# Kernel tuning notes

Hardware: AMD Instinct MI355X
Metric: run time of the kernel (lower is better)

Reference implementation:

```python
import jax, jax.numpy as jnp
import numpy as np

HEADS, DQK, DV = 4, 128, 128
HH, WW = 32, 32
SCALE = DQK ** -0.5
EPS = 1e-5


def bn(x, g, b, m, v):
    # eval-mode BatchNorm2d over channel dim of NCHW
    inv = g * jax.lax.rsqrt(v + EPS)
    return x * inv[:, None, None] + (b - m * inv)[:, None, None]


def rel_to_abs(x):
    # x: (B, Nh, L, 2L-1) -> (B, Nh, L, L)
    B, Nh, L, _ = x.shape
    x = jnp.pad(x, ((0, 0), (0, 0), (0, 0), (0, 1)))
    fx = x.reshape(B, Nh, L * 2 * L)
    fx = jnp.pad(fx, ((0, 0), (0, 0), (0, L - 1)))
    fx = fx.reshape(B, Nh, L + 1, 2 * L - 1)
    return fx[:, :, :L, L - 1:]


def rel_logits_1d(q, rel_k):
    # q: (B, Nh, H, W, D); rel_k: (2W-1, D)
    B, Nh, H, W, D = q.shape
    r = jnp.einsum('bnhwd,rd->bnhwr', q, rel_k)
    r = rel_to_abs(r.reshape(B, Nh * H, W, 2 * W - 1))
    r = r.reshape(B, Nh, H, W, W)
    return jnp.broadcast_to(r[:, :, :, None], (B, Nh, H, H, W, W))


def pos_bias(q, rel_h, rel_w):
    # q: (B, Nh, H*W, D), already scaled
    B, Nh, L, D = q.shape
    q5 = q.reshape(B, Nh, HH, WW, D)
    rw = rel_logits_1d(q5, rel_w)                     # (B,N,H,Hx,W,W)
    rw = rw.transpose(0, 1, 2, 4, 3, 5).reshape(B, Nh, HH * WW, HH * WW)
    rh = rel_logits_1d(q5.transpose(0, 1, 3, 2, 4), rel_h)  # (B,N,W,Wx,H,H)
    rh = rh.transpose(0, 1, 4, 2, 5, 3).reshape(B, Nh, HH * WW, HH * WW)
    return rw + rh


def to_heads(x):
    # (B, Nh*d, H, W) -> (B, Nh, H*W, d)
    B, C, H, W = x.shape
    x = x.reshape(B, HEADS, C // HEADS, H, W)
    return x.transpose(0, 1, 3, 4, 2).reshape(B, HEADS, H * W, C // HEADS)


def mhsa(x, w_qk, w_v, rel_h, rel_w):
    B, C, H, W = x.shape
    qk = jnp.einsum('bchw,oc->bohw', x, w_qk)
    q, k = jnp.split(qk, 2, axis=1)
    v = jnp.einsum('bchw,oc->bohw', x, w_v)
    q, k, v = to_heads(q), to_heads(k), to_heads(v)
    q = q * SCALE
    logits = jnp.einsum('bnid,bnjd->bnij', q, k) + pos_bias(q, rel_h, rel_w)
    weights = jax.nn.softmax(logits, axis=-1)
    out = jnp.einsum('bnij,bnjd->bnid', weights, v)   # (B,Nh,HW,dv)
    out = out.reshape(B, HEADS, H, W, DV).transpose(0, 1, 4, 2, 3)
    return out.reshape(B, HEADS * DV, H, W)


def setup_inputs() -> dict:
    key = jax.random.key(0)
    ks = jax.random.split(key, 12)
    d = {
        'x': jax.random.normal(ks[0], (8, 512, HH, WW), jnp.float32),
        'w_qk': jax.random.normal(ks[1], (2 * HEADS * DQK, 512), jnp.float32) * 0.02,
        'w_v': jax.random.normal(ks[2], (HEADS * DV, 512), jnp.float32) * 0.02,
        'rel_h': jax.random.normal(ks[3], (2 * HH - 1, DQK), jnp.float32) * SCALE,
        'rel_w': jax.random.normal(ks[4], (2 * WW - 1, DQK), jnp.float32) * SCALE,
        'g1': jnp.ones((512,), jnp.float32),
        'b1': jnp.zeros((512,), jnp.float32),
        'm1': jax.random.normal(ks[5], (512,), jnp.float32) * 0.1,
        'v1': jax.random.uniform(ks[6], (512,), jnp.float32) + 0.5,
        'g2': jnp.ones((512,), jnp.float32),
        'b2': jnp.zeros((512,), jnp.float32),
        'm2': jax.random.normal(ks[7], (512,), jnp.float32) * 0.1,
        'v2': jax.random.uniform(ks[8], (512,), jnp.float32) + 0.5,
        'w_fc': jax.random.normal(ks[9], (512, 512, 3, 3), jnp.float32) * 0.02,
        'bias_fc': jnp.zeros((512,), jnp.float32),
    }
    return d


def reference(x, w_qk, w_v, rel_h, rel_w, g1, b1, m1, v1, g2, b2, m2, v2, w_fc, bias_fc):
    out = jax.nn.relu(bn(x, g1, b1, m1, v1))
    out = mhsa(out, w_qk, w_v, rel_h, rel_w)
    x = out + x
    out = jax.nn.relu(bn(x, g2, b2, m2, v2))
    out = jax.lax.conv_general_dilated(
        out, w_fc, window_strides=(1, 1), padding='SAME',
        dimension_numbers=('NCHW', 'OIHW', 'NCHW')) + bias_fc[:, None, None]
    return out + x
```

## Files before the change

### kernel.cpp

```cpp
#include <hip/hip_runtime.h>

typedef __bf16 v8bf __attribute__((ext_vector_type(8)));
typedef float f32x4 __attribute__((ext_vector_type(4)));

#define DEVI static __device__ __forceinline__

DEVI v8bf load8(const __bf16* p) { return *reinterpret_cast<const v8bf*>(p); }

DEVI f32x4 mfma16(v8bf a, v8bf b, f32x4 c) {
  return __builtin_amdgcn_mfma_f32_16x16x32_bf16(a, b, c, 0, 0, 0);
}

DEVI void gld16(const __bf16* g, __bf16* l) {
  __builtin_amdgcn_global_load_lds(
      (const __attribute__((address_space(1))) unsigned int*)(const void*)g,
      (__attribute__((address_space(3))) unsigned int*)(void*)l, 16, 0, 0);
}

#define SCALE_Q 0.08838834764831845f

__global__ void k_prep(const float* __restrict__ wqk, const float* __restrict__ wv,
                       const float* __restrict__ relh, const float* __restrict__ relw,
                       const float* __restrict__ wfc, __bf16* __restrict__ wqkb,
                       __bf16* __restrict__ wvb, __bf16* __restrict__ rhb,
                       __bf16* __restrict__ rwb, __bf16* __restrict__ Wt,
                       float* __restrict__ zpad4) {
  const int bid = blockIdx.x, tid = threadIdx.x;
  if (bid < 2048) {
    int i = bid * 256 + tid;
    wqkb[i] = (__bf16)wqk[i];
  } else if (bid < 3072) {
    int i = (bid - 2048) * 256 + tid;
    wvb[i] = (__bf16)wv[i];
  } else if (bid < 3104) {
    int i = (bid - 3072) * 256 + tid;
    if (i < 8064) rhb[i] = (__bf16)relh[i];
  } else if (bid < 3136) {
    int i = (bid - 3104) * 256 + tid;
    if (i < 8064) rwb[i] = (__bf16)relw[i];
  } else if (bid < 4160) {
    int i = (bid - 3136) * 256 + tid;
    const float* src = wfc + (size_t)i * 9;
#pragma unroll
    for (int tap = 0; tap < 9; ++tap)
      Wt[(size_t)tap * 262144 + i] = (__bf16)src[tap];
  } else {
    int i = (bid - 4160) * 256 + tid;
    f32x4 z = {0.f, 0.f, 0.f, 0.f};
    reinterpret_cast<f32x4*>(zpad4)[i] = z;
  }
}

__global__ void k_bn1(const float* __restrict__ x, const float* __restrict__ g,
                      const float* __restrict__ bb, const float* __restrict__ m,
                      const float* __restrict__ v, __bf16* __restrict__ y) {
  __shared__ float tile[32][33];
  const int b = blockIdx.z, c0 = blockIdx.y * 32, s0 = blockIdx.x * 32;
  const int tx = threadIdx.x, ty = threadIdx.y;
#pragma unroll
  for (int r = 0; r < 4; ++r) {
    int c = c0 + ty + r * 8;
    float inv = g[c] * rsqrtf(v[c] + 1e-5f);
    float beta = bb[c] - m[c] * inv;
    float val = x[((size_t)b * 512 + c) * 1024 + s0 + tx] * inv + beta;
    tile[ty + r * 8][tx] = fmaxf(val, 0.0f);
  }
  __syncthreads();
#pragma unroll
  for (int r = 0; r < 4; ++r) {
    int s = s0 + ty + r * 8;
    y[((size_t)b * 1024 + s) * 512 + c0 + tx] = (__bf16)tile[tx][ty + r * 8];
  }
}

__global__ void k_bn2c(float* o0x2, const float* __restrict__ o1,
                       const float* __restrict__ lp, const float* __restrict__ xin,
                       const float* __restrict__ g, const float* __restrict__ bb,
                       const float* __restrict__ m, const float* __restrict__ v,
                       __bf16* __restrict__ zp) {
  __shared__ float tile[32][33];
  const int b = blockIdx.z, c0 = blockIdx.y * 32, s0 = blockIdx.x * 32;
  const int tx = threadIdx.x, ty = threadIdx.y;
  const int bnrow = b * 4 + (c0 >> 7);
  const int scol = s0 + tx;
  const float linv =
      1.0f / (lp[bnrow * 1024 + scol] + lp[32768 + bnrow * 1024 + scol]);
#pragma unroll
  for (int r = 0; r < 4; ++r) {
    int c = c0 + ty + r * 8;
    float inv = g[c] * rsqrtf(v[c] + 1e-5f);
    float beta = bb[c] - m[c] * inv;
    size_t idx = ((size_t)b * 512 + c) * 1024 + scol;
    float t = (o0x2[idx] + o1[idx]) * linv + xin[idx];
    o0x2[idx] = t;
    tile[ty + r * 8][tx] = fmaxf(t * inv + beta, 0.0f);
  }
  __syncthreads();
#pragma unroll
  for (int r = 0; r < 4; ++r) {
    int s = s0 + ty + r * 8;
    int hh = s >> 5, ww = s & 31;
    zp[(((size_t)b * 34 + hh + 1) * 34 + ww + 1) * 512 + c0 + tx] =
        (__bf16)tile[tx][ty + r * 8];
  }
}

__global__ __launch_bounds__(256) void k_proj(
    const __bf16* __restrict__ wall, const __bf16* __restrict__ y,
    __bf16* __restrict__ qout, __bf16* __restrict__ kout,
    __bf16* __restrict__ vout) {
  __shared__ __bf16 As[2][128 * 32];
  __shared__ __bf16 Bs[2][128 * 32];
  const int t = threadIdx.x;
  const int wave = t >> 6, lane = t & 63;
  const int l15 = lane & 15, quad = lane >> 4;
  const int mbase = blockIdx.x * 128;
  const int nbase = blockIdx.y * 128;
  const int mh = (wave >> 1) * 64, nh = (wave & 1) * 64;
  const bool isv = mbase >= 1024;

  const int row0 = t >> 2, part8 = (t & 3) * 8;
  const __bf16* gA0 = wall + (size_t)(mbase + row0) * 512 + part8;
  const __bf16* gA1 = gA0 + (size_t)64 * 512;
  const __bf16* gB0 = y + (size_t)(nbase + row0) * 512 + part8;
  const __bf16* gB1 = gB0 + (size_t)64 * 512;
  const int wofs = wave * 512;

  const f32x4 fz = {0.f, 0.f, 0.f, 0.f};
  f32x4 acc[4][4];
#pragma unroll
  for (int i = 0; i < 4; ++i)
#pragma unroll
    for (int j = 0; j < 4; ++j) acc[i][j] = fz;

  gld16(gA0, &As[0][wofs]);
  gld16(gA1, &As[0][2048 + wofs]);
  gld16(gB0, &Bs[0][wofs]);
  gld16(gB1, &Bs[0][2048 + wofs]);
  __syncthreads();

#pragma unroll 1
  for (int r = 0; r < 16; ++r) {
    const int cur = r & 1;
    if (r < 15) {
      const int kn = (r + 1) * 32;
      gld16(gA0 + kn, &As[cur ^ 1][wofs]);
      gld16(gA1 + kn, &As[cur ^ 1][2048 + wofs]);
      gld16(gB0 + kn, &Bs[cur ^ 1][wofs]);
      gld16(gB1 + kn, &Bs[cur ^ 1][2048 + wofs]);
    }
    v8bf a[4], bfr[4];
#pragma unroll
    for (int i = 0; i < 4; ++i)
      a[i] = load8(&As[cur][(mh + i * 16 + l15) * 32 + quad * 8]);
#pragma unroll
    for (int j = 0; j < 4; ++j)
      bfr[j] = load8(&Bs[cur][(nh + j * 16 + l15) * 32 + quad * 8]);
    if (isv) {
#pragma unroll
      for (int i = 0; i < 4; ++i)
#pragma unroll
        for (int j = 0; j < 4; ++j) acc[i][j] = mfma16(a[i], bfr[j], acc[i][j]);
    } else {
#pragma unroll
      for (int i = 0; i < 4; ++i)
#pragma unroll
        for (int j = 0; j < 4; ++j) acc[i][j] = mfma16(bfr[j], a[i], acc[i][j]);
    }
    __syncthreads();
  }

  if (isv) {
#pragma unroll
    for (int i = 0; i < 4; ++i)
#pragma unroll
      for (int j = 0; j < 4; ++j)
#pragma unroll
        for (int r = 0; r < 4; ++r) {
          int o = mbase + mh + i * 16 + quad * 4 + r;
          int nflat = nbase + nh + j * 16 + l15;
          int b = nflat >> 10, s = nflat & 1023;
          int oe = o - 1024; int n = oe >> 7, d = oe & 127;
          vout[(((size_t)b * 4 + n) * 128 + d) * 1024 + s] = (__bf16)acc[i][j][r];
        }
  } else {
    const bool isq = mbase < 512;
#pragma unroll
    for (int i = 0; i < 4; ++i)
#pragma unroll
      for (int j = 0; j < 4; ++j)
#pragma unroll
        for (int r = 0; r < 4; ++r) {
          int o = mbase + mh + i * 16 + l15;
          int nflat = nbase + nh + j * 16 + quad * 4 + r;
          int b = nflat >> 10, s = nflat & 1023;
          float val = acc[i][j][r];
          if (isq) {
            int n = o >> 7, d = o & 127;
            qout[(((size_t)b * 4 + n) * 1024 + s) * 128 + d] = (__bf16)(val * SCALE_Q);
          } else {
            int oe = o - 512; int n = oe >> 7, d = oe & 127;
            kout[(((size_t)b * 4 + n) * 1024 + s) * 128 + d] = (__bf16)val;
          }
        }
  }
}

__global__ __launch_bounds__(256, 2) void k_attn(
    const __bf16* __restrict__ q, const __bf16* __restrict__ kmat,
    const __bf16* __restrict__ vt, const __bf16* __restrict__ relh,
    const __bf16* __restrict__ relw, float* __restrict__ o0,
    float* __restrict__ o1, float* __restrict__ lpart) {
  __shared__ __bf16 Ks[32 * 128];
  __shared__ __bf16 Vs[128 * 32];
  __shared__ __bf16 P[4 * 32 * 36];
  __shared__ __bf16 RWs[128][33];
  __shared__ __bf16 RHs[128][33];

  const int Lb = blockIdx.x;
  const int xcd = Lb & 7, local = Lb >> 3;
  const int bn = xcd * 4 + (local & 3);
  const int qblk = (local >> 2) & 7;
  const int half = local >> 5;
  const int s0 = qblk * 128;

  const int t = threadIdx.x;
  const int wave = t >> 6, lane = t & 63;
  const int l15 = lane & 15, quad = lane >> 4;
  const size_t hoff = ((size_t)bn) << 17;
  const int s0w = s0 + wave * 32;
  const int h0w = s0w >> 5;
  const int j00 = half * 512;

  const __bf16* kgA =
      kmat + hoff + (size_t)((t >> 2) & 31) * 128 + (t >> 7) * 32 + (t & 3) * 8;
  const __bf16* vgA = vt + hoff + (size_t)(t >> 2) * 1024 + (t & 3) * 8;
  __bf16* kswA = Ks + wave * 512;
  __bf16* vswA = Vs + wave * 512;

#pragma unroll
  for (int c = 0; c < 2; ++c)
    gld16(kgA + (size_t)j00 * 128 + c * 64, kswA + c * 2048);
#pragma unroll
  for (int dh = 0; dh < 2; ++dh)
    gld16(vgA + (size_t)dh * 64 * 1024 + j00, vswA + dh * 2048);

  v8bf aq[2][4];
#pragma unroll
  for (int h = 0; h < 2; ++h) {
    const __bf16* qp = q + hoff + (size_t)(s0w + h * 16 + l15) * 128;
#pragma unroll
    for (int kk = 0; kk < 4; ++kk) aq[h][kk] = load8(qp + kk * 32 + quad * 8);
  }

#pragma unroll
  for (int h = 0; h < 2; ++h) {
#pragma unroll
    for (int nt = 0; nt < 4; ++nt) {
      int rr = nt * 16 + l15;
      const __bf16* bp = relw + (size_t)rr * 128;
      f32x4 acc = {0.f, 0.f, 0.f, 0.f};
#pragma unroll
      for (int kk = 0; kk < 4; ++kk)
        acc = mfma16(aq[h][kk], load8(bp + kk * 32 + quad * 8), acc);
#pragma unroll
      for (int r = 0; r < 4; ++r) {
        int row15 = quad * 4 + r;
        int wj = rr + h * 16 + row15 - 31;
        if (wj >= 0 && wj < 32)
          RWs[wave * 32 + h * 16 + row15][wj] = (__bf16)acc[r];
      }
    }
#pragma unroll
    for (int nt = 0; nt < 2; ++nt) {
      int hj = nt * 16 + l15;
      const __bf16* bp = relh + (size_t)(hj - h0w + 31) * 128;
      f32x4 acc = {0.f, 0.f, 0.f, 0.f};
#pragma unroll
      for (int kk = 0; kk < 4; ++kk)
        acc = mfma16(aq[h][kk], load8(bp + kk * 32 + quad * 8), acc);
#pragma unroll
      for (int r = 0; r < 4; ++r)
        RHs[wave * 32 + h * 16 + quad * 4 + r][hj] = (__bf16)acc[r];
    }
  }

  float rwreg[2][4][2];
#pragma unroll
  for (int h = 0; h < 2; ++h)
#pragma unroll
    for (int r = 0; r < 4; ++r) {
      const int gi = wave * 32 + h * 16 + quad * 4 + r;
      rwreg[h][r][0] = (float)RWs[gi][l15];
      rwreg[h][r][1] = (float)RWs[gi][l15 + 16];
    }

  __syncthreads();

  const f32x4 fz = {0.f, 0.f, 0.f, 0.f};
  float lsum[2][4];
#pragma unroll
  for (int h = 0; h < 2; ++h)
#pragma unroll
    for (int r = 0; r < 4; ++r) lsum[h][r] = 0.f;
  f32x4 oacc[2][8];
#pragma unroll
  for (int h = 0; h < 2; ++h)
#pragma unroll
    for (int dt = 0; dt < 8; ++dt) oacc[h][dt] = fz;
  __bf16* Pw = P + wave * 32 * 36;

#pragma unroll 1
  for (int iter = 0; iter < 16; ++iter) {
    asm volatile("s_waitcnt vmcnt(2)" ::: "memory");
    __builtin_amdgcn_s_barrier();
    __builtin_amdgcn_sched_barrier(0);

    v8bf kf[8];
#pragma unroll
    for (int nj = 0; nj < 2; ++nj)
#pragma unroll
      for (int kk = 0; kk < 4; ++kk)
        kf[nj * 4 + kk] =
            load8(&Ks[kk * 1024 + (nj * 16 + l15) * 32 + quad * 8]);

    f32x4 sacc[2][2];
    __builtin_amdgcn_s_setprio(1);
#pragma unroll
    for (int h = 0; h < 2; ++h)
#pragma unroll
      for (int nj = 0; nj < 2; ++nj) {
        f32x4 a = fz;
#pragma unroll
        for (int kk = 0; kk < 4; ++kk)
          a = mfma16(aq[h][kk], kf[nj * 4 + kk], a);
        sacc[h][nj] = a;
      }
    __builtin_amdgcn_s_setprio(0);

    const int hjb = half * 16 + iter;
#pragma unroll
    for (int h = 0; h < 2; ++h)
#pragma unroll
      for (int r = 0; r < 4; ++r) {
        const int row = h * 16 + quad * 4 + r;
        const float rh0 = (float)RHs[wave * 32 + row][hjb];
#pragma unroll
        for (int nj = 0; nj < 2; ++nj) {
          float val = sacc[h][nj][r] + rwreg[h][r][nj] + rh0;
          float p = __expf(fminf(val, 60.0f));
          lsum[h][r] += p;
          Pw[row * 36 + nj * 16 + l15] = (__bf16)p;
        }
      }
    v8bf pf[2];
#pragma unroll
    for (int h = 0; h < 2; ++h)
      pf[h] = *reinterpret_cast<const v8bf*>(&Pw[(h * 16 + l15) * 36 + quad * 8]);

    asm volatile("s_waitcnt vmcnt(0)" ::: "memory");
    __builtin_amdgcn_s_barrier();
    __builtin_amdgcn_sched_barrier(0);

    if (iter < 15) {
      const int jn = j00 + (iter + 1) * 32;
#pragma unroll
      for (int c = 0; c < 2; ++c)
        gld16(kgA + (size_t)jn * 128 + c * 64, kswA + c * 2048);
    }

    __builtin_amdgcn_s_setprio(1);
#pragma unroll
    for (int dt = 0; dt < 8; ++dt) {
      v8bf vf = load8(&Vs[(dt * 16 + l15) * 32 + quad * 8]);
#pragma unroll
      for (int h = 0; h < 2; ++h)
        oacc[h][dt] = mfma16(vf, pf[h], oacc[h][dt]);
    }
    __builtin_amdgcn_s_setprio(0);

    if (iter < 15) {
      asm volatile("s_waitcnt lgkmcnt(0)" ::: "memory");
      __builtin_amdgcn_s_barrier();
      __builtin_amdgcn_sched_barrier(0);
      const int jn = j00 + (iter + 1) * 32;
#pragma unroll
      for (int dh = 0; dh < 2; ++dh)
        gld16(vgA + (size_t)dh * 64 * 1024 + jn, vswA + dh * 2048);
    }
  }

#pragma unroll
  for (int h = 0; h < 2; ++h)
#pragma unroll
    for (int r = 0; r < 4; ++r) {
#pragma unroll
      for (int msk = 8; msk >= 1; msk >>= 1)
        lsum[h][r] += __shfl_xor(lsum[h][r], msk);
    }
  if (l15 == 0) {
#pragma unroll
    for (int h = 0; h < 2; ++h)
#pragma unroll
      for (int r = 0; r < 4; ++r)
        lpart[half * 32768 + bn * 1024 + s0w + h * 16 + quad * 4 + r] =
            lsum[h][r];
  }

  {
    float* op = half ? o1 : o0;
#pragma unroll
    for (int h = 0; h < 2; ++h) {
      const int s = s0w + h * 16 + l15;
#pragma unroll
      for (int dt = 0; dt < 8; ++dt)
#pragma unroll
        for (int r = 0; r < 4; ++r) {
          int d = dt * 16 + quad * 4 + r;
          op[((size_t)bn * 128 + d) * 1024 + s] = oacc[h][dt][r];
        }
    }
  }
}

__global__ __launch_bounds__(256, 2) void k_conv(
    const __bf16* __restrict__ Wt, const __bf16* __restrict__ zp,
    float* __restrict__ part) {
  __shared__ __bf16 As[4 * 128 * 32];
  __shared__ __bf16 Bs[4 * 128 * 32];
  const int t = threadIdx.x;
  const int wave = t >> 6, lane = t & 63;
  const int l15 = lane & 15, quad = lane >> 4;

  const int Lb = blockIdx.x;
  const int logical = (Lb & 7) * 64 + (Lb >> 3);
  const int combo = logical & 7;
  const int ot = combo >> 1, sp = combo & 1;
  const int nt = logical >> 3;
  const int mbase = ot * 128;
  const int nbase = nt * 128;
  const int cs = sp * 256;
  const int mh = (wave >> 1) * 64, nh = (wave & 1) * 64;

  const int row0 = t >> 2;
  const int part8 = (t & 3) * 8;
  const __bf16* gA0 = Wt + (size_t)(mbase + row0) * 512 + cs + part8;
  const __bf16* gA1 = gA0 + (size_t)64 * 512;
  const int n0 = nbase + row0;
  const int b0 = n0 >> 10, spn = n0 & 1023;
  const __bf16* gB0 =
      zp + ((size_t)(b0 * 34 + (spn >> 5) + 1) * 34 + (spn & 31) + 1) * 512 + cs + part8;
  const __bf16* gB1 = gB0 + (size_t)2 * 34 * 512;
  const int wofs = wave * 512;

  const f32x4 fz = {0.f, 0.f, 0.f, 0.f};
  f32x4 acc[4][4];
#pragma unroll
  for (int i = 0; i < 4; ++i)
#pragma unroll
    for (int j = 0; j < 4; ++j) acc[i][j] = fz;

#pragma unroll 1
  for (int tap = 0; tap < 9; ++tap) {
    const int dh = tap / 3 - 1, dw = tap % 3 - 1;
    const size_t aoff = (size_t)tap * 512 * 512;
    const int boff = (dh * 34 + dw) * 512;
#pragma unroll 1
    for (int k0 = 0; k0 < 256; k0 += 128) {
      __syncthreads();
#pragma unroll
      for (int c = 0; c < 4; ++c) {
        const int kq = k0 + c * 32;
        gld16(gA0 + aoff + kq, As + c * 4096 + wofs);
        gld16(gA1 + aoff + kq, As + c * 4096 + 2048 + wofs);
        gld16(gB0 + boff + kq, Bs + c * 4096 + wofs);
        gld16(gB1 + boff + kq, Bs + c * 4096 + 2048 + wofs);
      }
      __syncthreads();
#pragma unroll
      for (int c = 0; c < 4; ++c) {
        v8bf a[4], bfr[4];
#pragma unroll
        for (int i = 0; i < 4; ++i)
          a[i] = load8(&As[c * 4096 + (mh + i * 16 + l15) * 32 + quad * 8]);
#pragma unroll
        for (int j = 0; j < 4; ++j)
          bfr[j] = load8(&Bs[c * 4096 + (nh + j * 16 + l15) * 32 + quad * 8]);
#pragma unroll
        for (int i = 0; i < 4; ++i)
#pragma unroll
          for (int j = 0; j < 4; ++j) acc[i][j] = mfma16(a[i], bfr[j], acc[i][j]);
      }
    }
  }

  float* pout = part + (size_t)sp * 8 * 512 * 1024;
#pragma unroll
  for (int i = 0; i < 4; ++i)
#pragma unroll
    for (int j = 0; j < 4; ++j)
#pragma unroll
      for (int r = 0; r < 4; ++r) {
        int o = mbase + mh + i * 16 + quad * 4 + r;
        int nn = nbase + nh + j * 16 + l15;
        int bb2 = nn >> 10, s = nn & 1023;
        pout[((size_t)bb2 * 512 + o) * 1024 + s] = acc[i][j][r];
      }
}

__global__ void k_sum(const float* __restrict__ part, const float* __restrict__ bias,
                      const float* __restrict__ x2, float* __restrict__ out) {
  int i = blockIdx.x * 256 + threadIdx.x;
  int o = (i >> 8) & 511;
  f32x4 p0 = reinterpret_cast<const f32x4*>(part)[i];
  f32x4 p1 = reinterpret_cast<const f32x4*>(part + (size_t)8 * 512 * 1024)[i];
  f32x4 xr = reinterpret_cast<const f32x4*>(x2)[i];
  float bo = bias[o];
  f32x4 r;
#pragma unroll
  for (int c = 0; c < 4; ++c) r[c] = p0[c] + p1[c] + bo + xr[c];
  reinterpret_cast<f32x4*>(out)[i] = r;
}

extern "C" void kernel_launch(void* const* d_in, const int* in_sizes, int n_in,
                              void* d_out, int out_size, void* d_ws, size_t ws_size,
                              hipStream_t stream) {
  const float* x    = (const float*)d_in[0];
  const float* wqk  = (const float*)d_in[1];
  const float* wv   = (const float*)d_in[2];
  const float* relh = (const float*)d_in[3];
  const float* relw = (const float*)d_in[4];
  const float* g1   = (const float*)d_in[5];
  const float* b1   = (const float*)d_in[6];
  const float* m1   = (const float*)d_in[7];
  const float* v1   = (const float*)d_in[8];
  const float* g2   = (const float*)d_in[9];
  const float* b2   = (const float*)d_in[10];
  const float* m2   = (const float*)d_in[11];
  const float* v2   = (const float*)d_in[12];
  const float* wfc  = (const float*)d_in[13];
  const float* bfc  = (const float*)d_in[14];
  float* out = (float*)d_out;

  char* p = (char*)d_ws;
  __bf16* y    = (__bf16*)p; p += (size_t)8 * 1024 * 512 * 2;
  __bf16* qb   = (__bf16*)p; p += (size_t)8 * 4 * 1024 * 128 * 2;
  __bf16* kb   = (__bf16*)p; p += (size_t)8 * 4 * 1024 * 128 * 2;
  __bf16* vb   = (__bf16*)p; p += (size_t)8 * 4 * 1024 * 128 * 2;
  __bf16* Wt   = (__bf16*)p; p += (size_t)9 * 512 * 512 * 2;
  __bf16* wqkb = (__bf16*)p; p += (size_t)1024 * 512 * 2;
  __bf16* wvb  = (__bf16*)p; p += (size_t)512 * 512 * 2;
  __bf16* rhb  = (__bf16*)p; p += 32768;
  __bf16* rwb  = (__bf16*)p; p += 32768;
  float*  x2   = (float*)p;  p += (size_t)8 * 512 * 1024 * 4;
  __bf16* zpad = (__bf16*)p; p += (size_t)8 * 34 * 34 * 512 * 2;
  float* lpart = (float*)d_ws;
  float* o0 = x2;
  float* o1 = (float*)d_out;
  float* part = (float*)d_ws;

  k_prep<<<dim3(6472), dim3(256), 0, stream>>>(wqk, wv, relh, relw, wfc,
                                               wqkb, wvb, rhb, rwb, Wt, (float*)zpad);
  k_bn1<<<dim3(32, 16, 8), dim3(32, 8), 0, stream>>>(x, g1, b1, m1, v1, y);
  k_proj<<<dim3(12, 64), dim3(256), 0, stream>>>(wqkb, y, qb, kb, vb);
  k_attn<<<dim3(512), dim3(256), 0, stream>>>(qb, kb, vb, rhb, rwb, o0, o1, lpart);
  k_bn2c<<<dim3(32, 16, 8), dim3(32, 8), 0, stream>>>(o0, o1, lpart, x,
                                                      g2, b2, m2, v2, zpad);
  k_conv<<<dim3(512), dim3(256), 0, stream>>>(Wt, zpad, part);
  k_sum<<<dim3(4096), dim3(256), 0, stream>>>(part, bfc, x2, out);
}
```

Before: 242.7 us.

## Merge attention key-halves in one 512-thread block and fuse normalization plus residual

The attention kernel now runs both key halves in one 512-thread workgroup, as two groups of four waves. The halves are combined through shared memory, and the softmax normalization plus residual add are applied in the epilogue, which writes x2 directly. This removes the fp32 partial outputs o0/o1 and the lpart round trip, and it simplifies the bn2 kernel to a plain BN+ReLU transpose. In exchange the grid is halved, the block size doubles, shared memory grows, and extra barriers are needed for the cross-group reduction.

```diff
diff --git a/kernel.cpp b/kernel.cpp
--- a/kernel.cpp
+++ b/kernel.cpp
@@ -73,27 +73,19 @@
   }
 }
 
-__global__ void k_bn2c(float* o0x2, const float* __restrict__ o1,
-                       const float* __restrict__ lp, const float* __restrict__ xin,
-                       const float* __restrict__ g, const float* __restrict__ bb,
-                       const float* __restrict__ m, const float* __restrict__ v,
-                       __bf16* __restrict__ zp) {
+__global__ void k_bn2(const float* __restrict__ x2, const float* __restrict__ g,
+                      const float* __restrict__ bb, const float* __restrict__ m,
+                      const float* __restrict__ v, __bf16* __restrict__ zp) {
   __shared__ float tile[32][33];
   const int b = blockIdx.z, c0 = blockIdx.y * 32, s0 = blockIdx.x * 32;
   const int tx = threadIdx.x, ty = threadIdx.y;
-  const int bnrow = b * 4 + (c0 >> 7);
-  const int scol = s0 + tx;
-  const float linv =
-      1.0f / (lp[bnrow * 1024 + scol] + lp[32768 + bnrow * 1024 + scol]);
 #pragma unroll
   for (int r = 0; r < 4; ++r) {
     int c = c0 + ty + r * 8;
     float inv = g[c] * rsqrtf(v[c] + 1e-5f);
     float beta = bb[c] - m[c] * inv;
-    size_t idx = ((size_t)b * 512 + c) * 1024 + scol;
-    float t = (o0x2[idx] + o1[idx]) * linv + xin[idx];
-    o0x2[idx] = t;
-    tile[ty + r * 8][tx] = fmaxf(t * inv + beta, 0.0f);
+    float val = x2[((size_t)b * 512 + c) * 1024 + s0 + tx] * inv + beta;
+    tile[ty + r * 8][tx] = fmaxf(val, 0.0f);
   }
   __syncthreads();
 #pragma unroll
@@ -206,37 +198,41 @@
   }
 }
 
-__global__ __launch_bounds__(256, 2) void k_attn(
+__global__ __launch_bounds__(512, 2) void k_attn(
     const __bf16* __restrict__ q, const __bf16* __restrict__ kmat,
     const __bf16* __restrict__ vt, const __bf16* __restrict__ relh,
-    const __bf16* __restrict__ relw, float* __restrict__ o0,
-    float* __restrict__ o1, float* __restrict__ lpart) {
-  __shared__ __bf16 Ks[32 * 128];
-  __shared__ __bf16 Vs[128 * 32];
-  __shared__ __bf16 P[4 * 32 * 36];
-  __shared__ __bf16 RWs[128][33];
-  __shared__ __bf16 RHs[128][33];
+    const __bf16* __restrict__ relw, const float* __restrict__ x,
+    float* __restrict__ x2) {
+  __shared__ __attribute__((aligned(16))) char smem[58880];
+  __bf16* Ks = (__bf16*)smem;
+  __bf16* Vs = (__bf16*)(smem + 16384);
+  __bf16* P  = (__bf16*)(smem + 32768);
+  auto RWs = (__bf16(*)[33])(smem + 41984);
+  auto RHs = (__bf16(*)[33])(smem + 50432);
 
   const int Lb = blockIdx.x;
   const int xcd = Lb & 7, local = Lb >> 3;
   const int bn = xcd * 4 + (local & 3);
-  const int qblk = (local >> 2) & 7;
-  const int half = local >> 5;
+  const int qblk = local >> 2;
   const int s0 = qblk * 128;
 
   const int t = threadIdx.x;
   const int wave = t >> 6, lane = t & 63;
+  const int wg = wave >> 2, w4 = wave & 3;
+  const int tl = t & 255;
   const int l15 = lane & 15, quad = lane >> 4;
   const size_t hoff = ((size_t)bn) << 17;
-  const int s0w = s0 + wave * 32;
+  const int s0w = s0 + w4 * 32;
   const int h0w = s0w >> 5;
-  const int j00 = half * 512;
+  const int j00 = wg * 512;
 
   const __bf16* kgA =
-      kmat + hoff + (size_t)((t >> 2) & 31) * 128 + (t >> 7) * 32 + (t & 3) * 8;
-  const __bf16* vgA = vt + hoff + (size_t)(t >> 2) * 1024 + (t & 3) * 8;
-  __bf16* kswA = Ks + wave * 512;
-  __bf16* vswA = Vs + wave * 512;
+      kmat + hoff + (size_t)((tl >> 2) & 31) * 128 + (tl >> 7) * 32 + (tl & 3) * 8;
+  const __bf16* vgA = vt + hoff + (size_t)(tl >> 2) * 1024 + (tl & 3) * 8;
+  __bf16* kbase = Ks + wg * 4096;
+  __bf16* vbase = Vs + wg * 4096;
+  __bf16* kswA = kbase + w4 * 512;
+  __bf16* vswA = vbase + w4 * 512;
 
 #pragma unroll
   for (int c = 0; c < 2; ++c)
@@ -253,50 +249,52 @@
     for (int kk = 0; kk < 4; ++kk) aq[h][kk] = load8(qp + kk * 32 + quad * 8);
   }
 
-#pragma unroll
-  for (int h = 0; h < 2; ++h) {
-#pragma unroll
-    for (int nt = 0; nt < 4; ++nt) {
-      int rr = nt * 16 + l15;
-      const __bf16* bp = relw + (size_t)rr * 128;
-      f32x4 acc = {0.f, 0.f, 0.f, 0.f};
-#pragma unroll
-      for (int kk = 0; kk < 4; ++kk)
-        acc = mfma16(aq[h][kk], load8(bp + kk * 32 + quad * 8), acc);
-#pragma unroll
-      for (int r = 0; r < 4; ++r) {
-        int row15 = quad * 4 + r;
-        int wj = rr + h * 16 + row15 - 31;
-        if (wj >= 0 && wj < 32)
-          RWs[wave * 32 + h * 16 + row15][wj] = (__bf16)acc[r];
-      }
-    }
-#pragma unroll
-    for (int nt = 0; nt < 2; ++nt) {
-      int hj = nt * 16 + l15;
-      const __bf16* bp = relh + (size_t)(hj - h0w + 31) * 128;
-      f32x4 acc = {0.f, 0.f, 0.f, 0.f};
-#pragma unroll
-      for (int kk = 0; kk < 4; ++kk)
-        acc = mfma16(aq[h][kk], load8(bp + kk * 32 + quad * 8), acc);
-#pragma unroll
-      for (int r = 0; r < 4; ++r)
-        RHs[wave * 32 + h * 16 + quad * 4 + r][hj] = (__bf16)acc[r];
-    }
-  }
+  if (wg == 0) {
+#pragma unroll
+    for (int h = 0; h < 2; ++h) {
+#pragma unroll
+      for (int nt = 0; nt < 4; ++nt) {
+        int rr = nt * 16 + l15;
+        const __bf16* bp = relw + (size_t)rr * 128;
+        f32x4 acc = {0.f, 0.f, 0.f, 0.f};
+#pragma unroll
+        for (int kk = 0; kk < 4; ++kk)
+          acc = mfma16(aq[h][kk], load8(bp + kk * 32 + quad * 8), acc);
+#pragma unroll
+        for (int r = 0; r < 4; ++r) {
+          int row15 = quad * 4 + r;
+          int wj = rr + h * 16 + row15 - 31;
+          if (wj >= 0 && wj < 32)
+            RWs[w4 * 32 + h * 16 + row15][wj] = (__bf16)acc[r];
+        }
+      }
+#pragma unroll
+      for (int nt = 0; nt < 2; ++nt) {
+        int hj = nt * 16 + l15;
+        const __bf16* bp = relh + (size_t)(hj - h0w + 31) * 128;
+        f32x4 acc = {0.f, 0.f, 0.f, 0.f};
+#pragma unroll
+        for (int kk = 0; kk < 4; ++kk)
+          acc = mfma16(aq[h][kk], load8(bp + kk * 32 + quad * 8), acc);
+#pragma unroll
+        for (int r = 0; r < 4; ++r)
+          RHs[w4 * 32 + h * 16 + quad * 4 + r][hj] = (__bf16)acc[r];
+      }
+    }
+  }
+
+  __syncthreads();
 
   float rwreg[2][4][2];
 #pragma unroll
   for (int h = 0; h < 2; ++h)
 #pragma unroll
     for (int r = 0; r < 4; ++r) {
-      const int gi = wave * 32 + h * 16 + quad * 4 + r;
+      const int gi = w4 * 32 + h * 16 + quad * 4 + r;
       rwreg[h][r][0] = (float)RWs[gi][l15];
       rwreg[h][r][1] = (float)RWs[gi][l15 + 16];
     }
 
-  __syncthreads();
-
   const f32x4 fz = {0.f, 0.f, 0.f, 0.f};
   float lsum[2][4];
 #pragma unroll
@@ -308,7 +306,7 @@
   for (int h = 0; h < 2; ++h)
 #pragma unroll
     for (int dt = 0; dt < 8; ++dt) oacc[h][dt] = fz;
-  __bf16* Pw = P + wave * 32 * 36;
+  __bf16* Pw16 = P + wave * 16 * 36;
 
 #pragma unroll 1
   for (int iter = 0; iter < 16; ++iter) {
@@ -322,7 +320,7 @@
 #pragma unroll
       for (int kk = 0; kk < 4; ++kk)
         kf[nj * 4 + kk] =
-            load8(&Ks[kk * 1024 + (nj * 16 + l15) * 32 + quad * 8]);
+            load8(&kbase[kk * 1024 + (nj * 16 + l15) * 32 + quad * 8]);
 
     f32x4 sacc[2][2];
     __builtin_amdgcn_s_setprio(1);
@@ -338,25 +336,24 @@
       }
     __builtin_amdgcn_s_setprio(0);
 
-    const int hjb = half * 16 + iter;
-#pragma unroll
-    for (int h = 0; h < 2; ++h)
+    const int hjb = wg * 16 + iter;
+    v8bf pf[2];
+#pragma unroll
+    for (int h = 0; h < 2; ++h) {
 #pragma unroll
       for (int r = 0; r < 4; ++r) {
-        const int row = h * 16 + quad * 4 + r;
-        const float rh0 = (float)RHs[wave * 32 + row][hjb];
+        const int row15 = quad * 4 + r;
+        const float rh0 = (float)RHs[w4 * 32 + h * 16 + row15][hjb];
 #pragma unroll
         for (int nj = 0; nj < 2; ++nj) {
           float val = sacc[h][nj][r] + rwreg[h][r][nj] + rh0;
           float p = __expf(fminf(val, 60.0f));
           lsum[h][r] += p;
-          Pw[row * 36 + nj * 16 + l15] = (__bf16)p;
+          Pw16[row15 * 36 + nj * 16 + l15] = (__bf16)p;
         }
       }
-    v8bf pf[2];
-#pragma unroll
-    for (int h = 0; h < 2; ++h)
-      pf[h] = *reinterpret_cast<const v8bf*>(&Pw[(h * 16 + l15) * 36 + quad * 8]);
+      pf[h] = *reinterpret_cast<const v8bf*>(&Pw16[l15 * 36 + quad * 8]);
+    }
 
     asm volatile("s_waitcnt vmcnt(0)" ::: "memory");
     __builtin_amdgcn_s_barrier();
@@ -372,7 +369,7 @@
     __builtin_amdgcn_s_setprio(1);
 #pragma unroll
     for (int dt = 0; dt < 8; ++dt) {
-      v8bf vf = load8(&Vs[(dt * 16 + l15) * 32 + quad * 8]);
+      v8bf vf = load8(&vbase[(dt * 16 + l15) * 32 + quad * 8]);
 #pragma unroll
       for (int h = 0; h < 2; ++h)
         oacc[h][dt] = mfma16(vf, pf[h], oacc[h][dt]);
@@ -398,27 +395,56 @@
       for (int msk = 8; msk >= 1; msk >>= 1)
         lsum[h][r] += __shfl_xor(lsum[h][r], msk);
     }
-  if (l15 == 0) {
-#pragma unroll
-    for (int h = 0; h < 2; ++h)
-#pragma unroll
-      for (int r = 0; r < 4; ++r)
-        lpart[half * 32768 + bn * 1024 + s0w + h * 16 + quad * 4 + r] =
-            lsum[h][r];
-  }
-
-  {
-    float* op = half ? o1 : o0;
-#pragma unroll
-    for (int h = 0; h < 2; ++h) {
-      const int s = s0w + h * 16 + l15;
-#pragma unroll
-      for (int dt = 0; dt < 8; ++dt)
-#pragma unroll
-        for (int r = 0; r < 4; ++r) {
-          int d = dt * 16 + quad * 4 + r;
-          op[((size_t)bn * 128 + d) * 1024 + s] = oacc[h][dt][r];
+
+  float* xbuf = (float*)smem;
+  float* lb0 = (float*)(smem + 33792);
+  float* lb1 = lb0 + 64;
+
+#pragma unroll 1
+  for (int rnd = 0; rnd < 2; ++rnd) {
+    __syncthreads();
+    if ((w4 >> 1) == rnd) {
+      const int bA = w4 & 1;
+      if (wg == 1) {
+#pragma unroll
+        for (int h = 0; h < 2; ++h) {
+#pragma unroll
+          for (int dt = 0; dt < 8; ++dt)
+#pragma unroll
+            for (int r = 0; r < 4; ++r)
+              xbuf[(bA * 32 + h * 16 + l15) * 132 + dt * 16 + quad * 4 + r] =
+                  oacc[h][dt][r];
+          if (l15 == 0)
+#pragma unroll
+            for (int r = 0; r < 4; ++r)
+              lb1[bA * 32 + h * 16 + quad * 4 + r] = lsum[h][r];
         }
+      } else {
+        if (l15 == 0)
+#pragma unroll
+          for (int h = 0; h < 2; ++h)
+#pragma unroll
+            for (int r = 0; r < 4; ++r)
+              lb0[bA * 32 + h * 16 + quad * 4 + r] = lsum[h][r];
+      }
+    }
+    __syncthreads();
+    if (wg == 0 && (w4 >> 1) == rnd) {
+      const int bA = w4 & 1;
+#pragma unroll
+      for (int h = 0; h < 2; ++h) {
+        const int ri = bA * 32 + h * 16 + l15;
+        const float linv = 1.0f / (lb0[ri] + lb1[ri]);
+        const int s = s0w + h * 16 + l15;
+#pragma unroll
+        for (int dt = 0; dt < 8; ++dt)
+#pragma unroll
+          for (int r = 0; r < 4; ++r) {
+            int d = dt * 16 + quad * 4 + r;
+            size_t gi = ((size_t)bn * 128 + d) * 1024 + s;
+            x2[gi] = (oacc[h][dt][r] + xbuf[ri * 132 + d]) * linv + x[gi];
+          }
+      }
     }
   }
 }
@@ -554,18 +580,14 @@
   __bf16* rwb  = (__bf16*)p; p += 32768;
   float*  x2   = (float*)p;  p += (size_t)8 * 512 * 1024 * 4;
   __bf16* zpad = (__bf16*)p; p += (size_t)8 * 34 * 34 * 512 * 2;
-  float* lpart = (float*)d_ws;
-  float* o0 = x2;
-  float* o1 = (float*)d_out;
   float* part = (float*)d_ws;
 
   k_prep<<<dim3(6472), dim3(256), 0, stream>>>(wqk, wv, relh, relw, wfc,
                                                wqkb, wvb, rhb, rwb, Wt, (float*)zpad);
   k_bn1<<<dim3(32, 16, 8), dim3(32, 8), 0, stream>>>(x, g1, b1, m1, v1, y);
   k_proj<<<dim3(12, 64), dim3(256), 0, stream>>>(wqkb, y, qb, kb, vb);
-  k_attn<<<dim3(512), dim3(256), 0, stream>>>(qb, kb, vb, rhb, rwb, o0, o1, lpart);
-  k_bn2c<<<dim3(32, 16, 8), dim3(32, 8), 0, stream>>>(o0, o1, lpart, x,
-                                                      g2, b2, m2, v2, zpad);
+  k_attn<<<dim3(256), dim3(512), 0, stream>>>(qb, kb, vb, rhb, rwb, x, x2);
+  k_bn2<<<dim3(32, 16, 8), dim3(32, 8), 0, stream>>>(x2, g2, b2, m2, v2, zpad);
   k_conv<<<dim3(512), dim3(256), 0, stream>>>(Wt, zpad, part);
   k_sum<<<dim3(4096), dim3(256), 0, stream>>>(part, bfc, x2, out);
 }
```

After: 253.4 us. +4.4%, slower.
